# Performance work log

Measured on AMD Instinct MI355X. Metric: run time of the kernel, lower is better.

## Reference

```python
import math
import jax, jax.numpy as jnp
import numpy as np

EMBED = 512
HEADS = 8
EPS = 1e-5


def _ln(x, gamma, beta):
    mu = jnp.mean(x, axis=-1, keepdims=True)
    var = jnp.mean(jnp.square(x - mu), axis=-1, keepdims=True)
    return (x - mu) * jax.lax.rsqrt(var + EPS) * gamma + beta


def setup_inputs() -> dict:
    key = jax.random.key(0)
    ks = jax.random.split(key, 16)
    D = EMBED
    s = 0.02
    inp = {
        "moves_embeddings": jax.random.normal(ks[0], (4, 2048, D), dtype=jnp.float32),
        "wq": jax.random.normal(ks[1], (D, D), dtype=jnp.float32) * s,
        "bq": jnp.zeros((D,), jnp.float32),
        "wk": jax.random.normal(ks[2], (D, D), dtype=jnp.float32) * s,
        "bk": jnp.zeros((D,), jnp.float32),
        "wv": jax.random.normal(ks[3], (D, D), dtype=jnp.float32) * s,
        "bv": jnp.zeros((D,), jnp.float32),
        "wo": jax.random.normal(ks[4], (D, D), dtype=jnp.float32) * s,
        "bo": jnp.zeros((D,), jnp.float32),
        "w_up": jax.random.normal(ks[5], (D, 4 * D), dtype=jnp.float32) * s,
        "b_up": jnp.zeros((4 * D,), jnp.float32),
        "w_down": jax.random.normal(ks[6], (4 * D, D), dtype=jnp.float32) * s,
        "b_down": jnp.zeros((D,), jnp.float32),
        "g1": jnp.ones((D,), jnp.float32),
        "beta1": jnp.zeros((D,), jnp.float32),
        "g2": jnp.ones((D,), jnp.float32),
        "beta2": jnp.zeros((D,), jnp.float32),
    }
    return inp


def reference(moves_embeddings, wq, bq, wk, bk, wv, bv, wo, bo,
              w_up, b_up, w_down, b_down, g1, beta1, g2, beta2):
    x = moves_embeddings  # [B, S, D]
    B, S, D = x.shape
    Hd = D // HEADS
    # QKV projections, split heads -> [B, H, S, Hd]
    q = (x @ wq + bq).reshape(B, S, HEADS, Hd).transpose(0, 2, 1, 3)
    k = (x @ wk + bk).reshape(B, S, HEADS, Hd).transpose(0, 2, 1, 3)
    v = (x @ wv + bv).reshape(B, S, HEADS, Hd).transpose(0, 2, 1, 3)
    # NOTE: original scales by sqrt(embedding_dim), not sqrt(head_dim)
    scores = jnp.einsum('bhqd,bhkd->bhqk', q, k) / math.sqrt(D)
    attn = jax.nn.softmax(scores, axis=-1)
    ctx = jnp.einsum('bhqk,bhkd->bhqd', attn, v)
    ctx = ctx.transpose(0, 2, 1, 3).reshape(B, S, D)
    y = ctx @ wo + bo
    x = _ln(x + y, g1, beta1)
    # FFN with exact (erf) GELU, matching torch nn.GELU default
    h = jax.nn.gelu(x @ w_up + b_up, approximate=False)
    y = h @ w_down + b_down
    return _ln(x + y, g2, beta2)
```

## Files before the change

kernel.cpp:

```cpp
#include <hip/hip_runtime.h>
#include <math.h>

#define D 512
#define NHEADS 8
#define HD 64
#define SEQ 2048
#define BATCH 4
#define MROWS (BATCH*SEQ)
#define QKVSTR 1536
#define ATT_QSCALE 0.06376228841159383f

typedef short bf16x8 __attribute__((ext_vector_type(8)));
typedef float f32x4 __attribute__((ext_vector_type(4)));
typedef float f32x16 __attribute__((ext_vector_type(16)));

__device__ __forceinline__ ushort f2bf(float f) {
    union { float f; unsigned u; } v; v.f = f;
    unsigned r = (v.u + 0x7fffu + ((v.u >> 16) & 1u)) >> 16;
    return (ushort)r;
}
__device__ __forceinline__ float bf2f(ushort u) {
    union { unsigned u; float f; } v; v.u = ((unsigned)u) << 16; return v.f;
}

__device__ __forceinline__ unsigned cvt_pk_bf16(float lo, float hi_) {
    unsigned r;
    asm("v_cvt_pk_bf16_f32 %0, %1, %2" : "=v"(r) : "v"(lo), "v"(hi_));
    return r;
}

__device__ __forceinline__ float exp2_hw(float x) {
    float r;
    asm("v_exp_f32 %0, %1" : "=v"(r) : "v"(x));
    return r;
}
__device__ __forceinline__ float rcp_hw(float x) {
    float r;
    asm("v_rcp_f32 %0, %1" : "=v"(r) : "v"(x));
    return r;
}

__device__ __forceinline__ float gelu_fast(float x) {
    const float z = fabsf(x) * 0.70710678118654752f;
    const float t = rcp_hw(fmaf(0.3275911f, z, 1.0f));
    float p = fmaf(1.061405429f, t, -1.453152027f);
    p = fmaf(p, t, 1.421413741f);
    p = fmaf(p, t, -0.284496736f);
    p = fmaf(p, t, 0.254829592f);
    const float e = exp2_hw(-z * z * 1.4426950408889634f);
    const float erfz = 1.0f - p * t * e;
    const float s = copysignf(erfz, x);
    return 0.5f * x * (1.0f + s);
}

__device__ __forceinline__ void plswap(unsigned &a, unsigned &b) {
    asm("v_permlane32_swap_b32 %0, %1" : "+v"(a), "+v"(b));
}
__device__ __forceinline__ void plswapf(float &a, float &b) {
    union { float f; unsigned u; } ua, ub;
    ua.f = a; ub.f = b;
    asm("v_permlane32_swap_b32 %0, %1" : "+v"(ua.u), "+v"(ub.u));
    a = ua.f; b = ub.f;
}

__device__ __forceinline__ void gload16(const void* g, void* lds) {
    __builtin_amdgcn_global_load_lds(
        (const __attribute__((address_space(1))) unsigned int*)(uintptr_t)g,
        (__attribute__((address_space(3))) unsigned int*)(uintptr_t)lds,
        16, 0, 0);
}

__device__ __forceinline__ int xcd_swz(int wg, int nwg) {
    const int cpx = nwg >> 3;
    return (wg & 7) * cpx + (wg >> 3);
}

template<int GELU, int OBF16, int SPLITK>
__global__ __launch_bounds__(512)
void gemm_mfma8(const ushort* __restrict__ A, const ushort* __restrict__ Bt,
                const float* __restrict__ bias, void* __restrict__ Cp,
                void* __restrict__ Cp2, int M, int N, int K)
{
    __shared__ ushort As[2][128 * 64];
    __shared__ ushort Bs[2][128 * 64];

    const int tid = threadIdx.x;
    const int w = tid >> 6, lane = tid & 63;
    const int lr = lane & 15, lg = lane >> 4;
    const int wr = w >> 2, wc = w & 3;

    const int gx = gridDim.x;
    const int wg = xcd_swz(blockIdx.y * gx + blockIdx.x, gx * gridDim.y);
    const int row0 = (wg / gx) * 128, col0 = (wg % gx) * 128;

    const int kLen = SPLITK ? (K >> 1) : K;
    const int kOff = SPLITK ? blockIdx.z * kLen : 0;

    const int srow = lane >> 3;
    const int schunk = (lane & 7) ^ srow;

    const ushort* aSrc = A  + (size_t)(row0 + w * 16 + srow) * K + kOff + schunk * 8;
    const ushort* bSrc = Bt + (size_t)(col0 + w * 16 + srow) * K + kOff + schunk * 8;

    f32x4 acc[4][2] = {};

    auto STAGE = [&](int buf, int k0) {
        ushort* aD = &As[buf][(w * 16) * 64];
        ushort* bD = &Bs[buf][(w * 16) * 64];
        gload16(aSrc + k0,                 aD);
        gload16(aSrc + (size_t)8 * K + k0, aD + 8 * 64);
        gload16(bSrc + k0,                 bD);
        gload16(bSrc + (size_t)8 * K + k0, bD + 8 * 64);
    };

    auto COMPUTE = [&](int buf) {
        const ushort* AsB = As[buf];
        const ushort* BsB = Bs[buf];
        #pragma unroll
        for (int kc = 0; kc < 2; ++kc) {
            bf16x8 af[4], bfr[2];
            #pragma unroll
            for (int mt = 0; mt < 4; ++mt)
                af[mt] = *(const bf16x8*)&AsB[(wr * 64 + mt * 16 + lr) * 64 +
                                             (((kc * 4 + lg) ^ (lr & 7)) * 8)];
            #pragma unroll
            for (int nt = 0; nt < 2; ++nt)
                bfr[nt] = *(const bf16x8*)&BsB[(wc * 32 + nt * 16 + lr) * 64 +
                                              (((kc * 4 + lg) ^ (lr & 7)) * 8)];
            __builtin_amdgcn_s_setprio(1);
            #pragma unroll
            for (int mt = 0; mt < 4; ++mt)
                #pragma unroll
                for (int nt = 0; nt < 2; ++nt)
                    acc[mt][nt] = __builtin_amdgcn_mfma_f32_16x16x32_bf16(
                        af[mt], bfr[nt], acc[mt][nt], 0, 0, 0);
            __builtin_amdgcn_s_setprio(0);
        }
    };

    const int nk = kLen >> 6;
    STAGE(0, 0);
    __syncthreads();
    for (int t = 0; t < nk; ++t) {
        if (t + 1 < nk) STAGE((t + 1) & 1, (t + 1) << 6);
        COMPUTE(t & 1);
        __syncthreads();
    }

    float* Pp = SPLITK ? (blockIdx.z ? (float*)Cp2 : (float*)Cp) : (float*)Cp;
    #pragma unroll
    for (int nt = 0; nt < 2; ++nt) {
        const int col = col0 + wc * 32 + nt * 16 + lr;
        const float bv = SPLITK ? 0.f : bias[col];
        #pragma unroll
        for (int mt = 0; mt < 4; ++mt) {
            #pragma unroll
            for (int i = 0; i < 4; ++i) {
                float o = acc[mt][nt][i] + bv;
                if (GELU) o = gelu_fast(o);
                const size_t idx = (size_t)(row0 + wr * 64 + mt * 16 + lg * 4 + i) * N + col;
                if (OBF16) ((ushort*)Cp)[idx] = f2bf(o);
                else       Pp[idx] = o;
            }
        }
    }
}

__global__ __launch_bounds__(512)
void gemm_qkv8(const ushort* __restrict__ A, const ushort* __restrict__ Bt,
               const float* __restrict__ bias, ushort* __restrict__ qkv,
               ushort* __restrict__ vt)
{
    __shared__ ushort As[2][128 * 64];
    __shared__ ushort Bs[2][128 * 64];

    const int tid = threadIdx.x;
    const int w = tid >> 6, lane = tid & 63;
    const int lr = lane & 15, lg = lane >> 4;
    const int wr = w >> 2, wc = w & 3;

    const int gx = gridDim.x;
    const int wg = xcd_swz(blockIdx.y * gx + blockIdx.x, gx * gridDim.y);
    const int row0 = (wg / gx) * 128, col0 = (wg % gx) * 128;

    const int K = 512;

    const int srow = lane >> 3;
    const int schunk = (lane & 7) ^ srow;

    const ushort* aSrc = A  + (size_t)(row0 + w * 16 + srow) * K + schunk * 8;
    const ushort* bSrc = Bt + (size_t)(col0 + w * 16 + srow) * K + schunk * 8;

    f32x4 acc[4][2] = {};

    auto STAGE = [&](int buf, int k0) {
        ushort* aD = &As[buf][(w * 16) * 64];
        ushort* bD = &Bs[buf][(w * 16) * 64];
        gload16(aSrc + k0,                 aD);
        gload16(aSrc + (size_t)8 * K + k0, aD + 8 * 64);
        gload16(bSrc + k0,                 bD);
        gload16(bSrc + (size_t)8 * K + k0, bD + 8 * 64);
    };

    auto COMPUTE = [&](int buf) {
        const ushort* AsB = As[buf];
        const ushort* BsB = Bs[buf];
        #pragma unroll
        for (int kc = 0; kc < 2; ++kc) {
            bf16x8 af[4], bfr[2];
            #pragma unroll
            for (int mt = 0; mt < 4; ++mt)
                af[mt] = *(const bf16x8*)&AsB[(wr * 64 + mt * 16 + lr) * 64 +
                                             (((kc * 4 + lg) ^ (lr & 7)) * 8)];
            #pragma unroll
            for (int nt = 0; nt < 2; ++nt)
                bfr[nt] = *(const bf16x8*)&BsB[(wc * 32 + nt * 16 + lr) * 64 +
                                              (((kc * 4 + lg) ^ (lr & 7)) * 8)];
            __builtin_amdgcn_s_setprio(1);
            #pragma unroll
            for (int mt = 0; mt < 4; ++mt)
                #pragma unroll
                for (int nt = 0; nt < 2; ++nt)
                    acc[mt][nt] = __builtin_amdgcn_mfma_f32_16x16x32_bf16(
                        af[mt], bfr[nt], acc[mt][nt], 0, 0, 0);
            __builtin_amdgcn_s_setprio(0);
        }
    };

    STAGE(0, 0);
    __syncthreads();
    for (int t = 0; t < 8; ++t) {
        if (t + 1 < 8) STAGE((t + 1) & 1, (t + 1) << 6);
        COMPUTE(t & 1);
        __syncthreads();
    }

    #pragma unroll
    for (int nt = 0; nt < 2; ++nt) {
        const int col = col0 + wc * 32 + nt * 16 + lr;
        const float bv = bias[col];
        if (col < 1024) {
            const float sc = (col < 512) ? ATT_QSCALE : 1.0f;
            #pragma unroll
            for (int mt = 0; mt < 4; ++mt) {
                #pragma unroll
                for (int i = 0; i < 4; ++i) {
                    const float o = (acc[mt][nt][i] + bv) * sc;
                    qkv[(size_t)(row0 + wr * 64 + mt * 16 + lg * 4 + i) * QKVSTR + col] = f2bf(o);
                }
            }
        } else {
            const int hh = (col - 1024) >> 6, d = (col - 1024) & 63;
            #pragma unroll
            for (int mt = 0; mt < 4; ++mt) {
                const int rowb = row0 + wr * 64 + mt * 16 + lg * 4;
                const int bb = rowb >> 11, ss = rowb & (SEQ - 1);
                ushort4 o4;
                o4.x = f2bf(acc[mt][nt][0] + bv);
                o4.y = f2bf(acc[mt][nt][1] + bv);
                o4.z = f2bf(acc[mt][nt][2] + bv);
                o4.w = f2bf(acc[mt][nt][3] + bv);
                *(ushort4*)&vt[((size_t)(bb * NHEADS + hh) * HD + d) * SEQ + ss] = o4;
            }
        }
    }
}

#define KBLK 64
#define NKT (1024 / KBLK)

__global__ __launch_bounds__(512, 4)
void attn_mfma(const ushort* __restrict__ qkv, const ushort* __restrict__ vt,
               ushort* __restrict__ ctx)
{
    __shared__ __align__(16) ushort smem[2][2][2][64 * 64];

    const int tid = threadIdx.x;
    const int lane = tid & 63;
    const int l32 = lane & 31, hi = lane >> 5;
    const int w = tid >> 6;
    const int qsub = w & 3, half = w >> 2;

    const int flat = blockIdx.x + 16 * (blockIdx.y + 8 * blockIdx.z);
    const int wg = xcd_swz(flat, 512);
    const int qt = wg & 15, h = (wg >> 4) & 7, b = wg >> 7;

    const int q0 = qt * 128 + qsub * 32;
    const int kbase = half * 1024;

    const size_t seqbase = (size_t)b * SEQ;
    const ushort* Qp = qkv + (seqbase + q0 + l32) * QKVSTR + h * HD;
    const ushort* Kg = qkv + seqbase * QKVSTR + 512 + h * HD;
    const ushort* Vg = vt + (size_t)(b * NHEADS + h) * HD * SEQ;

    bf16x8 qf[4];
    #pragma unroll
    for (int c = 0; c < 4; ++c) qf[c] = *(const bf16x8*)&Qp[c * 16 + hi * 8];

    const int srow = lane >> 3;
    const int sslot  = (lane & 7) ^ srow;
    const int sslot2 = sslot ^ 1;
    const ushort* pK  = Kg + (size_t)(kbase + qsub * 16 + srow) * QKVSTR + sslot * 8;
    const ushort* pK2 = Kg + (size_t)(kbase + qsub * 16 + 8 + srow) * QKVSTR + sslot2 * 8;
    const ushort* pV  = Vg + (size_t)(qsub * 16 + srow) * SEQ + kbase + sslot * 8;
    const ushort* pV2 = Vg + (size_t)(qsub * 16 + 8 + srow) * SEQ + kbase + sslot2 * 8;

    const int pswz = (l32 & 7) ^ ((l32 >> 3) & 1);

    f32x16 o0 = {}, o1 = {};
    float l = 0.f;

    auto STAGE = [&](int buf) {
        ushort* dK = &smem[buf][half][0][(qsub * 16) * 64];
        ushort* dV = &smem[buf][half][1][(qsub * 16) * 64];
        gload16(pK,  dK);
        gload16(pK2, dK + 8 * 64);
        gload16(pV,  dV);
        gload16(pV2, dV + 8 * 64);
        pK  += (size_t)KBLK * QKVSTR;
        pK2 += (size_t)KBLK * QKVSTR;
        pV  += KBLK;
        pV2 += KBLK;
    };

    auto COMPUTE = [&](int buf) {
        const ushort* KsH = &smem[buf][half][0][0];
        const ushort* VsH = &smem[buf][half][1][0];

        f32x16 s0 = {}, s1 = {};

        __builtin_amdgcn_s_setprio(1);
        #pragma unroll
        for (int c = 0; c < 4; ++c) {
            const bf16x8 kf0 = *(const bf16x8*)&KsH[l32 * 64 + (((2 * c + hi) ^ pswz) * 8)];
            s0 = __builtin_amdgcn_mfma_f32_32x32x16_bf16(kf0, qf[c], s0, 0, 0, 0);
        }
        __builtin_amdgcn_s_setprio(0);

        #pragma unroll
        for (int c = 0; c < 4; ++c) {
            const bf16x8 kf1 = *(const bf16x8*)&KsH[(32 + l32) * 64 + (((2 * c + hi) ^ pswz) * 8)];
            s1 = __builtin_amdgcn_mfma_f32_32x32x16_bf16(kf1, qf[c], s1, 0, 0, 0);
        }

        float ts = 0.f;
        unsigned wp[16];
        union { unsigned u[4]; bf16x8 v; } pb[4];

        #pragma unroll
        for (int r = 0; r < 16; ++r) { s0[r] = exp2_hw(s0[r]); ts += s0[r]; }
        #pragma unroll
        for (int j = 0; j < 8; ++j) wp[j] = cvt_pk_bf16(s0[2 * j], s0[2 * j + 1]);
        plswap(wp[0], wp[2]);  plswap(wp[1], wp[3]);
        plswap(wp[4], wp[6]);  plswap(wp[5], wp[7]);
        pb[0].u[0] = wp[0]; pb[0].u[1] = wp[1]; pb[0].u[2] = wp[2]; pb[0].u[3] = wp[3];
        pb[1].u[0] = wp[4]; pb[1].u[1] = wp[5]; pb[1].u[2] = wp[6]; pb[1].u[3] = wp[7];

        #pragma unroll
        for (int kg = 0; kg < 2; ++kg) {
            const bf16x8 vf0 = *(const bf16x8*)&VsH[l32 * 64 + (((2 * kg + hi) ^ pswz) * 8)];
            o0 = __builtin_amdgcn_mfma_f32_32x32x16_bf16(vf0, pb[kg].v, o0, 0, 0, 0);
            const bf16x8 vf1 = *(const bf16x8*)&VsH[(32 + l32) * 64 + (((2 * kg + hi) ^ pswz) * 8)];
            o1 = __builtin_amdgcn_mfma_f32_32x32x16_bf16(vf1, pb[kg].v, o1, 0, 0, 0);
        }

        #pragma unroll
        for (int r = 0; r < 16; ++r) { s1[r] = exp2_hw(s1[r]); ts += s1[r]; }
        #pragma unroll
        for (int j = 0; j < 8; ++j) wp[8 + j] = cvt_pk_bf16(s1[2 * j], s1[2 * j + 1]);
        plswap(wp[8], wp[10]);  plswap(wp[9], wp[11]);
        plswap(wp[12], wp[14]); plswap(wp[13], wp[15]);
        pb[2].u[0] = wp[8];  pb[2].u[1] = wp[9];  pb[2].u[2] = wp[10]; pb[2].u[3] = wp[11];
        pb[3].u[0] = wp[12]; pb[3].u[1] = wp[13]; pb[3].u[2] = wp[14]; pb[3].u[3] = wp[15];

        #pragma unroll
        for (int kg = 2; kg < 4; ++kg) {
            const bf16x8 vf0 = *(const bf16x8*)&VsH[l32 * 64 + (((2 * kg + hi) ^ pswz) * 8)];
            o0 = __builtin_amdgcn_mfma_f32_32x32x16_bf16(vf0, pb[kg].v, o0, 0, 0, 0);
            const bf16x8 vf1 = *(const bf16x8*)&VsH[(32 + l32) * 64 + (((2 * kg + hi) ^ pswz) * 8)];
            o1 = __builtin_amdgcn_mfma_f32_32x32x16_bf16(vf1, pb[kg].v, o1, 0, 0, 0);
        }

        l += ts;
    };

    STAGE(0);
    __syncthreads();
    for (int tt = 0; tt < NKT; tt += 2) {
        if (tt + 1 < NKT) STAGE(1);
        COMPUTE(0);
        __syncthreads();
        if (tt + 2 < NKT) STAGE(0);
        COMPUTE(1);
        __syncthreads();
    }

    { float a_ = l, b_ = l; plswapf(a_, b_); l = a_ + b_; }

    float* so = (float*)smem;
    float* sl = (float*)((char*)smem + 4 * 64 * 33 * 4);
    if (half) {
        float* row = so + (qsub * 64 + lane) * 33;
        #pragma unroll
        for (int r = 0; r < 16; ++r) row[r] = o0[r];
        #pragma unroll
        for (int r = 0; r < 16; ++r) row[16 + r] = o1[r];
        sl[qsub * 64 + lane] = l;
    }
    __syncthreads();
    if (!half) {
        const float lb = sl[qsub * 64 + lane];
        const float* row = so + (qsub * 64 + lane) * 33;
        const float inv = 1.f / (l + lb);

        ushort* dst = ctx + (seqbase + q0 + l32) * D + h * HD;
        #pragma unroll
        for (int g = 0; g < 4; ++g) {
            ushort4 t0, t1;
            t0.x = f2bf((o0[g * 4 + 0] + row[g * 4 + 0]) * inv);
            t0.y = f2bf((o0[g * 4 + 1] + row[g * 4 + 1]) * inv);
            t0.z = f2bf((o0[g * 4 + 2] + row[g * 4 + 2]) * inv);
            t0.w = f2bf((o0[g * 4 + 3] + row[g * 4 + 3]) * inv);
            t1.x = f2bf((o1[g * 4 + 0] + row[16 + g * 4 + 0]) * inv);
            t1.y = f2bf((o1[g * 4 + 1] + row[16 + g * 4 + 1]) * inv);
            t1.z = f2bf((o1[g * 4 + 2] + row[16 + g * 4 + 2]) * inv);
            t1.w = f2bf((o1[g * 4 + 3] + row[16 + g * 4 + 3]) * inv);
            *(ushort4*)&dst[g * 8 + hi * 4]      = t0;
            *(ushort4*)&dst[32 + g * 8 + hi * 4] = t1;
        }
    }
}

template<int RESBF, int OUTBF>
__global__ __launch_bounds__(256)
void add_ln3(const void* __restrict__ res, const float* __restrict__ b0,
             const float* __restrict__ b1, const float* __restrict__ bias,
             const float* __restrict__ g, const float* __restrict__ beta,
             float* __restrict__ outf, ushort* __restrict__ outb)
{
    const int wave = threadIdx.x >> 6, lane = threadIdx.x & 63;
    const size_t row = (size_t)blockIdx.x * 4 + wave;

    float xr[8];
    if (RESBF) {
        const ushort* pr = (const ushort*)res + row * D + lane * 8;
        const ushort4 r0 = *(const ushort4*)pr;
        const ushort4 r1 = *(const ushort4*)(pr + 4);
        xr[0] = bf2f(r0.x); xr[1] = bf2f(r0.y); xr[2] = bf2f(r0.z); xr[3] = bf2f(r0.w);
        xr[4] = bf2f(r1.x); xr[5] = bf2f(r1.y); xr[6] = bf2f(r1.z); xr[7] = bf2f(r1.w);
    } else {
        const float* pr = (const float*)res + row * D + lane * 8;
        const float4 r0 = *(const float4*)pr;
        const float4 r1 = *(const float4*)(pr + 4);
        xr[0] = r0.x; xr[1] = r0.y; xr[2] = r0.z; xr[3] = r0.w;
        xr[4] = r1.x; xr[5] = r1.y; xr[6] = r1.z; xr[7] = r1.w;
    }

    const float* p0 = &b0[row * D + lane * 8];
    const float* p1 = &b1[row * D + lane * 8];
    const float4 c0 = *(const float4*)p0;
    const float4 c1 = *(const float4*)(p0 + 4);
    const float4 d0 = *(const float4*)p1;
    const float4 d1 = *(const float4*)(p1 + 4);
    const float4 bb0 = *(const float4*)&bias[lane * 8];
    const float4 bb1 = *(const float4*)&bias[lane * 8 + 4];

    float x[8];
    x[0] = xr[0] + c0.x + d0.x + bb0.x; x[1] = xr[1] + c0.y + d0.y + bb0.y;
    x[2] = xr[2] + c0.z + d0.z + bb0.z; x[3] = xr[3] + c0.w + d0.w + bb0.w;
    x[4] = xr[4] + c1.x + d1.x + bb1.x; x[5] = xr[5] + c1.y + d1.y + bb1.y;
    x[6] = xr[6] + c1.z + d1.z + bb1.z; x[7] = xr[7] + c1.w + d1.w + bb1.w;

    float sum = 0.f;
    #pragma unroll
    for (int i = 0; i < 8; ++i) sum += x[i];
    #pragma unroll
    for (int off = 32; off >= 1; off >>= 1) sum += __shfl_xor(sum, off);
    const float mu = sum * (1.0f / D);

    float vsum = 0.f;
    #pragma unroll
    for (int i = 0; i < 8; ++i) { const float dxe = x[i] - mu; vsum += dxe * dxe; }
    #pragma unroll
    for (int off = 32; off >= 1; off >>= 1) vsum += __shfl_xor(vsum, off);
    const float rs = rsqrtf(vsum * (1.0f / D) + 1e-5f);

    const float4 g0  = *(const float4*)&g[lane * 8];
    const float4 g1v = *(const float4*)&g[lane * 8 + 4];
    const float4 be0 = *(const float4*)&beta[lane * 8];
    const float4 be1 = *(const float4*)&beta[lane * 8 + 4];

    float o[8];
    o[0] = (x[0] - mu) * rs * g0.x  + be0.x;
    o[1] = (x[1] - mu) * rs * g0.y  + be0.y;
    o[2] = (x[2] - mu) * rs * g0.z  + be0.z;
    o[3] = (x[3] - mu) * rs * g0.w  + be0.w;
    o[4] = (x[4] - mu) * rs * g1v.x + be1.x;
    o[5] = (x[5] - mu) * rs * g1v.y + be1.y;
    o[6] = (x[6] - mu) * rs * g1v.z + be1.z;
    o[7] = (x[7] - mu) * rs * g1v.w + be1.w;

    if (OUTBF) {
        ushort4 lo, hi;
        lo.x = f2bf(o[0]); lo.y = f2bf(o[1]); lo.z = f2bf(o[2]); lo.w = f2bf(o[3]);
        hi.x = f2bf(o[4]); hi.y = f2bf(o[5]); hi.z = f2bf(o[6]); hi.w = f2bf(o[7]);
        ushort* pq = &outb[row * D + lane * 8];
        *(ushort4*)pq       = lo;
        *(ushort4*)(pq + 4) = hi;
    } else {
        float* po = &outf[row * D + lane * 8];
        *(float4*)po       = *(float4*)&o[0];
        *(float4*)(po + 4) = *(float4*)&o[4];
    }
}

__global__ __launch_bounds__(256)
void prep(const float* __restrict__ x, ushort* __restrict__ x_bf,
          const float* __restrict__ wq, const float* __restrict__ wk,
          const float* __restrict__ wv, const float* __restrict__ wo,
          const float* __restrict__ w_up, const float* __restrict__ w_down,
          ushort* __restrict__ Wt_qkv, ushort* __restrict__ Wt_o,
          ushort* __restrict__ Wt_up, ushort* __restrict__ Wt_down,
          const float* __restrict__ bq, const float* __restrict__ bk,
          const float* __restrict__ bv, float* __restrict__ b_qkv)
{
    const int bid = blockIdx.x;
    const int tid = threadIdx.x;

    if (bid < 2048) {
        const int i = bid * 256 + tid;
        const float4 a = *(const float4*)&x[(size_t)i * 8];
        const float4 b = *(const float4*)&x[(size_t)i * 8 + 4];
        ushort4 lo, hi;
        lo.x = f2bf(a.x); lo.y = f2bf(a.y); lo.z = f2bf(a.z); lo.w = f2bf(a.w);
        hi.x = f2bf(b.x); hi.y = f2bf(b.y); hi.z = f2bf(b.z); hi.w = f2bf(b.w);
        *(ushort4*)&x_bf[(size_t)i * 8]     = lo;
        *(ushort4*)&x_bf[(size_t)i * 8 + 4] = hi;
        return;
    }

    if (bid < 5120) {
        __shared__ float t[32][33];
        const int j = bid - 2048;
        const float* W; ushort* Wt; int N, stride, tI;
        if (j < 256)       { W = wq;     Wt = Wt_qkv;              N = 512;  stride = 512;  tI = j; }
        else if (j < 512)  { W = wk;     Wt = Wt_qkv + 512 * 512;  N = 512;  stride = 512;  tI = j - 256; }
        else if (j < 768)  { W = wv;     Wt = Wt_qkv + 1024 * 512; N = 512;  stride = 512;  tI = j - 512; }
        else if (j < 1024) { W = wo;     Wt = Wt_o;                N = 512;  stride = 512;  tI = j - 768; }
        else if (j < 2048) { W = w_up;   Wt = Wt_up;               N = 2048; stride = 512;  tI = j - 1024; }
        else               { W = w_down; Wt = Wt_down;             N = 512;  stride = 2048; tI = j - 2048; }
        const int ntn = N >> 5;
        const int n0 = (tI % ntn) * 32, k0 = (tI / ntn) * 32;
        const int r = tid >> 5, c = tid & 31;
        #pragma unroll
        for (int i = 0; i < 4; ++i)
            t[r + i * 8][c] = W[(size_t)(k0 + r + i * 8) * N + n0 + c];
        __syncthreads();
        #pragma unroll
        for (int i = 0; i < 4; ++i)
            Wt[(size_t)(n0 + r + i * 8) * stride + k0 + c] = f2bf(t[c][r + i * 8]);
        return;
    }

    const int i = (bid - 5120) * 256 + tid;
    if (i < 1536)
        b_qkv[i] = (i < 512) ? bq[i] : (i < 1024 ? bk[i - 512] : bv[i - 1024]);
}

extern "C" void kernel_launch(void* const* d_in, const int* in_sizes, int n_in,
                              void* d_out, int out_size, void* d_ws, size_t ws_size,
                              hipStream_t stream)
{
    const float* x      = (const float*)d_in[0];
    const float* wq     = (const float*)d_in[1];
    const float* bq     = (const float*)d_in[2];
    const float* wk     = (const float*)d_in[3];
    const float* bk     = (const float*)d_in[4];
    const float* wv     = (const float*)d_in[5];
    const float* bv     = (const float*)d_in[6];
    const float* wo     = (const float*)d_in[7];
    const float* bo     = (const float*)d_in[8];
    const float* w_up   = (const float*)d_in[9];
    const float* b_up   = (const float*)d_in[10];
    const float* w_down = (const float*)d_in[11];
    const float* b_down = (const float*)d_in[12];
    const float* g1     = (const float*)d_in[13];
    const float* beta1  = (const float*)d_in[14];
    const float* g2     = (const float*)d_in[15];
    const float* beta2  = (const float*)d_in[16];
    float* out = (float*)d_out;

    char* wsb = (char*)d_ws;
    #define WS(ofs_mb) (wsb + ((size_t)(ofs_mb) << 20))
    ushort* Wt_qkv  = (ushort*)WS(0);
    ushort* Wt_o    = (ushort*)WS(2);
    ushort* Wt_up   = (ushort*)WS(3);
    ushort* Wt_down = (ushort*)WS(5);
    float*  b_qkv   = (float*) WS(7);
    ushort* x_bf    = (ushort*)WS(8);
    ushort* qkv_bf  = (ushort*)WS(16);
    ushort* vt_bf   = (ushort*)WS(40);
    ushort* ctx_bf  = (ushort*)WS(48);
    float*  yp0     = (float*) WS(8);
    float*  yp1     = (float*) WS(24);
    ushort* x1_bf   = (ushort*)WS(40);
    ushort* h_bf    = (ushort*)WS(8);
    float*  y2p0    = (float*) WS(64);
    float*  y2p1    = (float*) WS(80);
    #undef WS

    const dim3 blk(256), blk8(512);

    prep<<<dim3(5126), blk, 0, stream>>>(x, x_bf, wq, wk, wv, wo, w_up, w_down,
                                         Wt_qkv, Wt_o, Wt_up, Wt_down,
                                         bq, bk, bv, b_qkv);

    gemm_qkv8<<<dim3(12, 64), blk8, 0, stream>>>(x_bf, Wt_qkv, b_qkv, qkv_bf, vt_bf);

    attn_mfma<<<dim3(SEQ / 128, NHEADS, BATCH), blk8, 0, stream>>>(qkv_bf, vt_bf, ctx_bf);

    gemm_mfma8<0, 0, 1><<<dim3(4, 64, 2), blk8, 0, stream>>>(ctx_bf, Wt_o, nullptr, yp0, yp1, MROWS, 512, 512);
    add_ln3<0, 1><<<dim3(MROWS / 4), blk, 0, stream>>>(x, yp0, yp1, bo, g1, beta1, nullptr, x1_bf);

    gemm_mfma8<1, 1, 0><<<dim3(16, 64), blk8, 0, stream>>>(x1_bf, Wt_up, b_up, h_bf, nullptr, MROWS, 2048, 512);
    gemm_mfma8<0, 0, 1><<<dim3(4, 64, 2), blk8, 0, stream>>>(h_bf, Wt_down, nullptr, y2p0, y2p1, MROWS, 512, 2048);
    add_ln3<1, 0><<<dim3(MROWS / 4), blk, 0, stream>>>(x1_bf, y2p0, y2p1, b_down, g2, beta2, out, nullptr);
}
```

Before: 148.5 us.

## Replace split-K N=512 GEMMs with 128x64-tile GEMM and single-partial LayerNorm

```diff
diff --git a/kernel.cpp b/kernel.cpp
--- a/kernel.cpp
+++ b/kernel.cpp
@@ -75,11 +75,11 @@
     return (wg & 7) * cpx + (wg >> 3);
 }
 
-template<int GELU, int OBF16, int SPLITK>
+template<int GELU, int OBF16>
 __global__ __launch_bounds__(512)
 void gemm_mfma8(const ushort* __restrict__ A, const ushort* __restrict__ Bt,
                 const float* __restrict__ bias, void* __restrict__ Cp,
-                void* __restrict__ Cp2, int M, int N, int K)
+                int M, int N, int K)
 {
     __shared__ ushort As[2][128 * 64];
     __shared__ ushort Bs[2][128 * 64];
@@ -93,14 +93,11 @@
     const int wg = xcd_swz(blockIdx.y * gx + blockIdx.x, gx * gridDim.y);
     const int row0 = (wg / gx) * 128, col0 = (wg % gx) * 128;
 
-    const int kLen = SPLITK ? (K >> 1) : K;
-    const int kOff = SPLITK ? blockIdx.z * kLen : 0;
-
     const int srow = lane >> 3;
     const int schunk = (lane & 7) ^ srow;
 
-    const ushort* aSrc = A  + (size_t)(row0 + w * 16 + srow) * K + kOff + schunk * 8;
-    const ushort* bSrc = Bt + (size_t)(col0 + w * 16 + srow) * K + kOff + schunk * 8;
+    const ushort* aSrc = A  + (size_t)(row0 + w * 16 + srow) * K + schunk * 8;
+    const ushort* bSrc = Bt + (size_t)(col0 + w * 16 + srow) * K + schunk * 8;
 
     f32x4 acc[4][2] = {};
 
@@ -138,7 +135,7 @@
         }
     };
 
-    const int nk = kLen >> 6;
+    const int nk = K >> 6;
     STAGE(0, 0);
     __syncthreads();
     for (int t = 0; t < nk; ++t) {
@@ -147,11 +144,10 @@
         __syncthreads();
     }
 
-    float* Pp = SPLITK ? (blockIdx.z ? (float*)Cp2 : (float*)Cp) : (float*)Cp;
     #pragma unroll
     for (int nt = 0; nt < 2; ++nt) {
         const int col = col0 + wc * 32 + nt * 16 + lr;
-        const float bv = SPLITK ? 0.f : bias[col];
+        const float bv = bias[col];
         #pragma unroll
         for (int mt = 0; mt < 4; ++mt) {
             #pragma unroll
@@ -160,7 +156,86 @@
                 if (GELU) o = gelu_fast(o);
                 const size_t idx = (size_t)(row0 + wr * 64 + mt * 16 + lg * 4 + i) * N + col;
                 if (OBF16) ((ushort*)Cp)[idx] = f2bf(o);
-                else       Pp[idx] = o;
+                else       ((float*)Cp)[idx] = o;
+            }
+        }
+    }
+}
+
+__global__ __launch_bounds__(512)
+void gemm_n64(const ushort* __restrict__ A, const ushort* __restrict__ Bt,
+              float* __restrict__ Y, int N, int K)
+{
+    __shared__ ushort As[2][128 * 64];
+    __shared__ ushort Bs[2][64 * 64];
+
+    const int tid = threadIdx.x;
+    const int w = tid >> 6, lane = tid & 63;
+    const int lr = lane & 15, lg = lane >> 4;
+    const int wr = w >> 1, wc = w & 1;
+
+    const int gx = gridDim.x;
+    const int wg = xcd_swz(blockIdx.y * gx + blockIdx.x, gx * gridDim.y);
+    const int row0 = (wg / gx) * 128, col0 = (wg % gx) * 64;
+
+    const int srow = lane >> 3;
+    const int schunk = (lane & 7) ^ srow;
+
+    const ushort* aSrc = A  + (size_t)(row0 + w * 16 + srow) * K + schunk * 8;
+    const ushort* bSrc = Bt + (size_t)(col0 + w * 8 + srow) * K + schunk * 8;
+
+    f32x4 acc[2][2] = {};
+
+    auto STAGE = [&](int buf, int k0) {
+        ushort* aD = &As[buf][(w * 16) * 64];
+        gload16(aSrc + k0,                 aD);
+        gload16(aSrc + (size_t)8 * K + k0, aD + 8 * 64);
+        gload16(bSrc + k0, &Bs[buf][(w * 8) * 64]);
+    };
+
+    auto COMPUTE = [&](int buf) {
+        const ushort* AsB = As[buf];
+        const ushort* BsB = Bs[buf];
+        #pragma unroll
+        for (int kc = 0; kc < 2; ++kc) {
+            bf16x8 af[2], bfr[2];
+            #pragma unroll
+            for (int mt = 0; mt < 2; ++mt)
+                af[mt] = *(const bf16x8*)&AsB[(wr * 32 + mt * 16 + lr) * 64 +
+                                             (((kc * 4 + lg) ^ (lr & 7)) * 8)];
+            #pragma unroll
+            for (int nt = 0; nt < 2; ++nt)
+                bfr[nt] = *(const bf16x8*)&BsB[(wc * 32 + nt * 16 + lr) * 64 +
+                                              (((kc * 4 + lg) ^ (lr & 7)) * 8)];
+            __builtin_amdgcn_s_setprio(1);
+            #pragma unroll
+            for (int mt = 0; mt < 2; ++mt)
+                #pragma unroll
+                for (int nt = 0; nt < 2; ++nt)
+                    acc[mt][nt] = __builtin_amdgcn_mfma_f32_16x16x32_bf16(
+                        af[mt], bfr[nt], acc[mt][nt], 0, 0, 0);
+            __builtin_amdgcn_s_setprio(0);
+        }
+    };
+
+    const int nk = K >> 6;
+    STAGE(0, 0);
+    __syncthreads();
+    for (int t = 0; t < nk; ++t) {
+        if (t + 1 < nk) STAGE((t + 1) & 1, (t + 1) << 6);
+        COMPUTE(t & 1);
+        __syncthreads();
+    }
+
+    #pragma unroll
+    for (int nt = 0; nt < 2; ++nt) {
+        const int col = col0 + wc * 32 + nt * 16 + lr;
+        #pragma unroll
+        for (int mt = 0; mt < 2; ++mt) {
+            #pragma unroll
+            for (int i = 0; i < 4; ++i) {
+                const size_t idx = (size_t)(row0 + wr * 32 + mt * 16 + lg * 4 + i) * N + col;
+                Y[idx] = acc[mt][nt][i];
             }
         }
     }
@@ -433,8 +508,8 @@
 
 template<int RESBF, int OUTBF>
 __global__ __launch_bounds__(256)
-void add_ln3(const void* __restrict__ res, const float* __restrict__ b0,
-             const float* __restrict__ b1, const float* __restrict__ bias,
+void add_ln2(const void* __restrict__ res, const float* __restrict__ y,
+             const float* __restrict__ bias,
              const float* __restrict__ g, const float* __restrict__ beta,
              float* __restrict__ outf, ushort* __restrict__ outb)
 {
@@ -456,20 +531,17 @@
         xr[4] = r1.x; xr[5] = r1.y; xr[6] = r1.z; xr[7] = r1.w;
     }
 
-    const float* p0 = &b0[row * D + lane * 8];
-    const float* p1 = &b1[row * D + lane * 8];
+    const float* p0 = &y[row * D + lane * 8];
     const float4 c0 = *(const float4*)p0;
     const float4 c1 = *(const float4*)(p0 + 4);
-    const float4 d0 = *(const float4*)p1;
-    const float4 d1 = *(const float4*)(p1 + 4);
     const float4 bb0 = *(const float4*)&bias[lane * 8];
     const float4 bb1 = *(const float4*)&bias[lane * 8 + 4];
 
     float x[8];
-    x[0] = xr[0] + c0.x + d0.x + bb0.x; x[1] = xr[1] + c0.y + d0.y + bb0.y;
-    x[2] = xr[2] + c0.z + d0.z + bb0.z; x[3] = xr[3] + c0.w + d0.w + bb0.w;
-    x[4] = xr[4] + c1.x + d1.x + bb1.x; x[5] = xr[5] + c1.y + d1.y + bb1.y;
-    x[6] = xr[6] + c1.z + d1.z + bb1.z; x[7] = xr[7] + c1.w + d1.w + bb1.w;
+    x[0] = xr[0] + c0.x + bb0.x; x[1] = xr[1] + c0.y + bb0.y;
+    x[2] = xr[2] + c0.z + bb0.z; x[3] = xr[3] + c0.w + bb0.w;
+    x[4] = xr[4] + c1.x + bb1.x; x[5] = xr[5] + c1.y + bb1.y;
+    x[6] = xr[6] + c1.z + bb1.z; x[7] = xr[7] + c1.w + bb1.w;
 
     float sum = 0.f;
     #pragma unroll
@@ -601,12 +673,10 @@
     ushort* qkv_bf  = (ushort*)WS(16);
     ushort* vt_bf   = (ushort*)WS(40);
     ushort* ctx_bf  = (ushort*)WS(48);
-    float*  yp0     = (float*) WS(8);
-    float*  yp1     = (float*) WS(24);
+    float*  y1      = (float*) WS(8);
     ushort* x1_bf   = (ushort*)WS(40);
     ushort* h_bf    = (ushort*)WS(8);
-    float*  y2p0    = (float*) WS(64);
-    float*  y2p1    = (float*) WS(80);
+    float*  y2      = (float*) WS(64);
     #undef WS
 
     const dim3 blk(256), blk8(512);
@@ -619,10 +689,10 @@
 
     attn_mfma<<<dim3(SEQ / 128, NHEADS, BATCH), blk8, 0, stream>>>(qkv_bf, vt_bf, ctx_bf);
 
-    gemm_mfma8<0, 0, 1><<<dim3(4, 64, 2), blk8, 0, stream>>>(ctx_bf, Wt_o, nullptr, yp0, yp1, MROWS, 512, 512);
-    add_ln3<0, 1><<<dim3(MROWS / 4), blk, 0, stream>>>(x, yp0, yp1, bo, g1, beta1, nullptr, x1_bf);
-
-    gemm_mfma8<1, 1, 0><<<dim3(16, 64), blk8, 0, stream>>>(x1_bf, Wt_up, b_up, h_bf, nullptr, MROWS, 2048, 512);
-    gemm_mfma8<0, 0, 1><<<dim3(4, 64, 2), blk8, 0, stream>>>(h_bf, Wt_down, nullptr, y2p0, y2p1, MROWS, 512, 2048);
-    add_ln3<1, 0><<<dim3(MROWS / 4), blk, 0, stream>>>(x1_bf, y2p0, y2p1, b_down, g2, beta2, out, nullptr);
-}
+    gemm_n64<<<dim3(8, 64), blk8, 0, stream>>>(ctx_bf, Wt_o, y1, 512, 512);
+    add_ln2<0, 1><<<dim3(MROWS / 4), blk, 0, stream>>>(x, y1, bo, g1, beta1, nullptr, x1_bf);
+
+    gemm_mfma8<1, 1><<<dim3(16, 64), blk8, 0, stream>>>(x1_bf, Wt_up, b_up, h_bf, MROWS, 2048, 512);
+    gemm_n64<<<dim3(8, 64), blk8, 0, stream>>>(h_bf, Wt_down, y2, 512, 2048);
+    add_ln2<1, 0><<<dim3(MROWS / 4), blk, 0, stream>>>(x1_bf, y2, b_down, g2, beta2, out, nullptr);
+}
```

After: 144.2 us, median of 2. 2.9% less time.

## Replace split-K 128x128 GEMMs with 128x64 tiles and single-pass add-LN

Applied to the files above, without the earlier changes.

```diff
diff --git a/kernel.cpp b/kernel.cpp
--- a/kernel.cpp
+++ b/kernel.cpp
@@ -75,42 +75,37 @@
     return (wg & 7) * cpx + (wg >> 3);
 }
 
-template<int GELU, int OBF16, int SPLITK>
+template<int GELU, int OBF16>
 __global__ __launch_bounds__(512)
-void gemm_mfma8(const ushort* __restrict__ A, const ushort* __restrict__ Bt,
-                const float* __restrict__ bias, void* __restrict__ Cp,
-                void* __restrict__ Cp2, int M, int N, int K)
+void gemm_n64(const ushort* __restrict__ A, const ushort* __restrict__ Bt,
+              const float* __restrict__ bias, void* __restrict__ Cp,
+              int N, int K)
 {
     __shared__ ushort As[2][128 * 64];
-    __shared__ ushort Bs[2][128 * 64];
+    __shared__ ushort Bs[2][64 * 64];
 
     const int tid = threadIdx.x;
     const int w = tid >> 6, lane = tid & 63;
     const int lr = lane & 15, lg = lane >> 4;
-    const int wr = w >> 2, wc = w & 3;
+    const int wr = w >> 1, wc = w & 1;
 
     const int gx = gridDim.x;
     const int wg = xcd_swz(blockIdx.y * gx + blockIdx.x, gx * gridDim.y);
-    const int row0 = (wg / gx) * 128, col0 = (wg % gx) * 128;
-
-    const int kLen = SPLITK ? (K >> 1) : K;
-    const int kOff = SPLITK ? blockIdx.z * kLen : 0;
+    const int row0 = (wg / gx) * 128, col0 = (wg % gx) * 64;
 
     const int srow = lane >> 3;
     const int schunk = (lane & 7) ^ srow;
 
-    const ushort* aSrc = A  + (size_t)(row0 + w * 16 + srow) * K + kOff + schunk * 8;
-    const ushort* bSrc = Bt + (size_t)(col0 + w * 16 + srow) * K + kOff + schunk * 8;
-
-    f32x4 acc[4][2] = {};
+    const ushort* aSrc = A  + (size_t)(row0 + w * 16 + srow) * K + schunk * 8;
+    const ushort* bSrc = Bt + (size_t)(col0 + w * 8 + srow) * K + schunk * 8;
+
+    f32x4 acc[2][2] = {};
 
     auto STAGE = [&](int buf, int k0) {
         ushort* aD = &As[buf][(w * 16) * 64];
-        ushort* bD = &Bs[buf][(w * 16) * 64];
         gload16(aSrc + k0,                 aD);
         gload16(aSrc + (size_t)8 * K + k0, aD + 8 * 64);
-        gload16(bSrc + k0,                 bD);
-        gload16(bSrc + (size_t)8 * K + k0, bD + 8 * 64);
+        gload16(bSrc + k0, &Bs[buf][(w * 8) * 64]);
     };
 
     auto COMPUTE = [&](int buf) {
@@ -118,10 +113,10 @@
         const ushort* BsB = Bs[buf];
         #pragma unroll
         for (int kc = 0; kc < 2; ++kc) {
-            bf16x8 af[4], bfr[2];
-            #pragma unroll
-            for (int mt = 0; mt < 4; ++mt)
-                af[mt] = *(const bf16x8*)&AsB[(wr * 64 + mt * 16 + lr) * 64 +
+            bf16x8 af[2], bfr[2];
+            #pragma unroll
+            for (int mt = 0; mt < 2; ++mt)
+                af[mt] = *(const bf16x8*)&AsB[(wr * 32 + mt * 16 + lr) * 64 +
                                              (((kc * 4 + lg) ^ (lr & 7)) * 8)];
             #pragma unroll
             for (int nt = 0; nt < 2; ++nt)
@@ -129,7 +124,7 @@
                                               (((kc * 4 + lg) ^ (lr & 7)) * 8)];
             __builtin_amdgcn_s_setprio(1);
             #pragma unroll
-            for (int mt = 0; mt < 4; ++mt)
+            for (int mt = 0; mt < 2; ++mt)
                 #pragma unroll
                 for (int nt = 0; nt < 2; ++nt)
                     acc[mt][nt] = __builtin_amdgcn_mfma_f32_16x16x32_bf16(
@@ -138,7 +133,7 @@
         }
     };
 
-    const int nk = kLen >> 6;
+    const int nk = K >> 6;
     STAGE(0, 0);
     __syncthreads();
     for (int t = 0; t < nk; ++t) {
@@ -147,20 +142,19 @@
         __syncthreads();
     }
 
-    float* Pp = SPLITK ? (blockIdx.z ? (float*)Cp2 : (float*)Cp) : (float*)Cp;
     #pragma unroll
     for (int nt = 0; nt < 2; ++nt) {
         const int col = col0 + wc * 32 + nt * 16 + lr;
-        const float bv = SPLITK ? 0.f : bias[col];
-        #pragma unroll
-        for (int mt = 0; mt < 4; ++mt) {
+        const float bv = OBF16 ? bias[col] : 0.f;
+        #pragma unroll
+        for (int mt = 0; mt < 2; ++mt) {
             #pragma unroll
             for (int i = 0; i < 4; ++i) {
                 float o = acc[mt][nt][i] + bv;
                 if (GELU) o = gelu_fast(o);
-                const size_t idx = (size_t)(row0 + wr * 64 + mt * 16 + lg * 4 + i) * N + col;
+                const size_t idx = (size_t)(row0 + wr * 32 + mt * 16 + lg * 4 + i) * N + col;
                 if (OBF16) ((ushort*)Cp)[idx] = f2bf(o);
-                else       Pp[idx] = o;
+                else       ((float*)Cp)[idx] = o;
             }
         }
     }
@@ -433,8 +427,8 @@
 
 template<int RESBF, int OUTBF>
 __global__ __launch_bounds__(256)
-void add_ln3(const void* __restrict__ res, const float* __restrict__ b0,
-             const float* __restrict__ b1, const float* __restrict__ bias,
+void add_ln2(const void* __restrict__ res, const float* __restrict__ y,
+             const float* __restrict__ bias,
              const float* __restrict__ g, const float* __restrict__ beta,
              float* __restrict__ outf, ushort* __restrict__ outb)
 {
@@ -456,20 +450,17 @@
         xr[4] = r1.x; xr[5] = r1.y; xr[6] = r1.z; xr[7] = r1.w;
     }
 
-    const float* p0 = &b0[row * D + lane * 8];
-    const float* p1 = &b1[row * D + lane * 8];
+    const float* p0 = &y[row * D + lane * 8];
     const float4 c0 = *(const float4*)p0;
     const float4 c1 = *(const float4*)(p0 + 4);
-    const float4 d0 = *(const float4*)p1;
-    const float4 d1 = *(const float4*)(p1 + 4);
     const float4 bb0 = *(const float4*)&bias[lane * 8];
     const float4 bb1 = *(const float4*)&bias[lane * 8 + 4];
 
     float x[8];
-    x[0] = xr[0] + c0.x + d0.x + bb0.x; x[1] = xr[1] + c0.y + d0.y + bb0.y;
-    x[2] = xr[2] + c0.z + d0.z + bb0.z; x[3] = xr[3] + c0.w + d0.w + bb0.w;
-    x[4] = xr[4] + c1.x + d1.x + bb1.x; x[5] = xr[5] + c1.y + d1.y + bb1.y;
-    x[6] = xr[6] + c1.z + d1.z + bb1.z; x[7] = xr[7] + c1.w + d1.w + bb1.w;
+    x[0] = xr[0] + c0.x + bb0.x; x[1] = xr[1] + c0.y + bb0.y;
+    x[2] = xr[2] + c0.z + bb0.z; x[3] = xr[3] + c0.w + bb0.w;
+    x[4] = xr[4] + c1.x + bb1.x; x[5] = xr[5] + c1.y + bb1.y;
+    x[6] = xr[6] + c1.z + bb1.z; x[7] = xr[7] + c1.w + bb1.w;
 
     float sum = 0.f;
     #pragma unroll
@@ -601,12 +592,10 @@
     ushort* qkv_bf  = (ushort*)WS(16);
     ushort* vt_bf   = (ushort*)WS(40);
     ushort* ctx_bf  = (ushort*)WS(48);
-    float*  yp0     = (float*) WS(8);
-    float*  yp1     = (float*) WS(24);
+    float*  y1      = (float*) WS(8);
     ushort* x1_bf   = (ushort*)WS(40);
     ushort* h_bf    = (ushort*)WS(8);
-    float*  y2p0    = (float*) WS(64);
-    float*  y2p1    = (float*) WS(80);
+    float*  y2      = (float*) WS(64);
     #undef WS
 
     const dim3 blk(256), blk8(512);
@@ -619,10 +608,10 @@
 
     attn_mfma<<<dim3(SEQ / 128, NHEADS, BATCH), blk8, 0, stream>>>(qkv_bf, vt_bf, ctx_bf);
 
-    gemm_mfma8<0, 0, 1><<<dim3(4, 64, 2), blk8, 0, stream>>>(ctx_bf, Wt_o, nullptr, yp0, yp1, MROWS, 512, 512);
-    add_ln3<0, 1><<<dim3(MROWS / 4), blk, 0, stream>>>(x, yp0, yp1, bo, g1, beta1, nullptr, x1_bf);
-
-    gemm_mfma8<1, 1, 0><<<dim3(16, 64), blk8, 0, stream>>>(x1_bf, Wt_up, b_up, h_bf, nullptr, MROWS, 2048, 512);
-    gemm_mfma8<0, 0, 1><<<dim3(4, 64, 2), blk8, 0, stream>>>(h_bf, Wt_down, nullptr, y2p0, y2p1, MROWS, 512, 2048);
-    add_ln3<1, 0><<<dim3(MROWS / 4), blk, 0, stream>>>(x1_bf, y2p0, y2p1, b_down, g2, beta2, out, nullptr);
-}
+    gemm_n64<0, 0><<<dim3(8, 64), blk8, 0, stream>>>(ctx_bf, Wt_o, nullptr, y1, 512, 512);
+    add_ln2<0, 1><<<dim3(MROWS / 4), blk, 0, stream>>>(x, y1, bo, g1, beta1, nullptr, x1_bf);
+
+    gemm_n64<1, 1><<<dim3(32, 64), blk8, 0, stream>>>(x1_bf, Wt_up, b_up, h_bf, 2048, 512);
+    gemm_n64<0, 0><<<dim3(8, 64), blk8, 0, stream>>>(h_bf, Wt_down, nullptr, y2, 512, 2048);
+    add_ln2<1, 0><<<dim3(MROWS / 4), blk, 0, stream>>>(x1_bf, y2, b_down, g2, beta2, out, nullptr);
+}
```

Result: no change. 146.3 us (-1.5%).
